# Kernel tuning notes

Hardware: AMD Instinct MI355X
Metric: run time of the kernel (lower is better)

Reference implementation:

```python
import jax, jax.numpy as jnp
import numpy as np

NVFP4_VALUES = jnp.array([0.0, 0.5, 1.0, 1.5, 2.0, 3.0, 4.0, 6.0], dtype=jnp.float32)
NVFP4_MAX = 6.0


def quantize_to_nvfp4(t):
    """Fake-quantize to NVFP4 (e2m1) via nearest codebook magnitude.
    Returns (quantized_tensor, inv_scale) matching the torch reference."""
    amax = jnp.maximum(jnp.max(jnp.abs(t)), 1e-12)
    scale = NVFP4_MAX / amax                      # scalar
    scaled = jnp.clip(t.astype(jnp.float32) * scale, -NVFP4_MAX, NVFP4_MAX)
    signs = jnp.sign(scaled)
    # distance to each of the 8 e2m1 magnitudes -> nearest index
    dist = jnp.abs(jnp.abs(scaled)[..., None] - NVFP4_VALUES)  # (..., 8)
    idx = jnp.argmin(dist, axis=-1)
    quantized = signs * NVFP4_VALUES[idx]
    return quantized, 1.0 / scale


def setup_inputs() -> dict:
    key = jax.random.key(0)
    kx, kw = jax.random.split(key)
    x = jax.random.normal(kx, (512, 4096), dtype=jnp.float32)          # batch=512 (in SUPPORTED_BATCH_SIZES -> no padding)
    # kaiming-uniform-ish init for weight [out_features, in_features]
    bound = float(np.sqrt(6.0 / 4096.0))
    weight = jax.random.uniform(kw, (4096, 4096), dtype=jnp.float32,
                                minval=-bound, maxval=bound)
    return {"x": x, "weight": weight}


def reference(x, weight):
    # batch==512 is an exact supported size, so pad/unpad is identity.
    x_q, x_inv_scale = quantize_to_nvfp4(x)
    w_q, w_inv_scale = quantize_to_nvfp4(weight)
    # out[b,o] = sum_i (x_q*x_s)[b,i] * (w_q*w_s)[o,i]
    out = jnp.einsum('bi,oi->bo', x_q * x_inv_scale, w_q * w_inv_scale)
    return out.astype(x.dtype)
```

## Files before the change

### kernel.cpp

```cpp
#include <hip/hip_runtime.h>

#define M_DIM 512
#define N_DIM 4096
#define K_DIM 4096

typedef __attribute__((ext_vector_type(4))) float f32x4;
typedef __attribute__((ext_vector_type(8))) int i32x8;
typedef __attribute__((ext_vector_type(4))) int i32x4;

#define PART_X_OFF 0
#define PART_X_N   256
#define PART_W_OFF 256
#define PART_W_N   1024
#define AMAX_OFF   1280
#define XQ_BYTE_OFF 8192
#define WQ_BYTE_OFF (XQ_BYTE_OFF + M_DIM * K_DIM)

__global__ __launch_bounds__(256) void amax_kernel(
    const float4* __restrict__ x4, const float4* __restrict__ w4,
    float* __restrict__ ws_f) {
    const int b = blockIdx.x;
    float m = 0.0f;
    if (b < PART_X_N) {
        const int n4 = M_DIM * K_DIM / 4, stride = PART_X_N * 256;
        for (int i = b * 256 + threadIdx.x; i < n4; i += stride) {
            float4 a = x4[i];
            m = fmaxf(m, fmaxf(fmaxf(fabsf(a.x), fabsf(a.y)),
                               fmaxf(fabsf(a.z), fabsf(a.w))));
        }
    } else {
        const int n4 = N_DIM * K_DIM / 4, stride = PART_W_N * 256;
        for (int i = (b - PART_X_N) * 256 + threadIdx.x; i < n4; i += stride) {
            float4 a = w4[i];
            m = fmaxf(m, fmaxf(fmaxf(fabsf(a.x), fabsf(a.y)),
                               fmaxf(fabsf(a.z), fabsf(a.w))));
        }
    }
    for (int off = 32; off > 0; off >>= 1)
        m = fmaxf(m, __shfl_down(m, off, 64));
    __shared__ float sm[4];
    if ((threadIdx.x & 63) == 0) sm[threadIdx.x >> 6] = m;
    __syncthreads();
    if (threadIdx.x == 0) {
        m = fmaxf(fmaxf(sm[0], sm[1]), fmaxf(sm[2], sm[3]));
        ws_f[(b < PART_X_N) ? (PART_X_OFF + b) : (PART_W_OFF + b - PART_X_N)] = m;
    }
}

__device__ __forceinline__ unsigned int q1(float x, float s) {
    float a = fabsf(x) * s;
    unsigned int b;
    if      (a <= 0.25f) b = 0x00u;
    else if (a <= 0.75f) b = 0x30u;
    else if (a <= 1.25f) b = 0x38u;
    else if (a <= 1.75f) b = 0x3Cu;
    else if (a <= 2.5f)  b = 0x40u;
    else if (a <= 3.5f)  b = 0x44u;
    else if (a <= 5.0f)  b = 0x48u;
    else                 b = 0x4Cu;
    return b | ((__float_as_uint(x) >> 24) & 0x80u);
}
__device__ __forceinline__ unsigned int qpack4(float4 v, float s) {
    return q1(v.x, s) | (q1(v.y, s) << 8) | (q1(v.z, s) << 16) | (q1(v.w, s) << 24);
}

__global__ __launch_bounds__(256) void quant_kernel(
    const float4* __restrict__ x4, const float4* __restrict__ w4,
    float* __restrict__ ws_f, unsigned char* __restrict__ ws_b) {
    const int b = blockIdx.x, t = threadIdx.x;
    const bool is_x = b < 512;
    float m = 0.0f;
    if (is_x) {
        m = ws_f[PART_X_OFF + t];
    } else {
        for (int i = t; i < PART_W_N; i += 256)
            m = fmaxf(m, ws_f[PART_W_OFF + i]);
    }
    for (int off = 32; off > 0; off >>= 1)
        m = fmaxf(m, __shfl_down(m, off, 64));
    __shared__ float sm[4];
    if ((t & 63) == 0) sm[t >> 6] = m;
    __syncthreads();
    m = fmaxf(fmaxf(sm[0], sm[1]), fmaxf(sm[2], sm[3]));
    float amax = fmaxf(m, 1e-12f);
    float s = 6.0f / amax;
    if (t == 0 && b == 0)   ws_f[AMAX_OFF + 0] = amax;
    if (t == 0 && b == 512) ws_f[AMAX_OFF + 1] = amax;

    const float4* src = is_x ? x4 : w4;
    unsigned char* dstb = ws_b + (is_x ? XQ_BYTE_OFF : WQ_BYTE_OFF);
    const int idx16 = (is_x ? b : b - 512) * 256 + t;
    const float4* p = src + (size_t)idx16 * 4;
    uint4 o;
    o.x = qpack4(p[0], s);
    o.y = qpack4(p[1], s);
    o.z = qpack4(p[2], s);
    o.w = qpack4(p[3], s);
    ((uint4*)dstb)[idx16] = o;
}

__device__ __forceinline__ void async_copy16(const void* g, void* l) {
    __builtin_amdgcn_global_load_lds(
        (const __attribute__((address_space(1))) unsigned int*)g,
        (__attribute__((address_space(3))) unsigned int*)l, 16, 0, 0);
}

__device__ __forceinline__ i32x8 frag_load(const unsigned char* rowbase,
                                           int mask, int g0) {
    const i32x4 lo = *(const i32x4*)(rowbase + ((g0 ^ mask) * 16));
    const i32x4 hi = *(const i32x4*)(rowbase + (((g0 + 1) ^ mask) * 16));
    return __builtin_shufflevector(lo, hi, 0, 1, 2, 3, 4, 5, 6, 7);
}

__global__ __launch_bounds__(256, 2) void gemm_kernel(
    const unsigned char* __restrict__ A, const unsigned char* __restrict__ B,
    float* __restrict__ C, const float* __restrict__ amax2) {
    __shared__ __align__(16) unsigned char As[64 * 512];
    __shared__ __align__(16) unsigned char Bs[64 * 512];

    const int bid  = blockIdx.x;
    const int bm   = (bid >> 6) * 64;
    const int bn   = ((bid & 7) * 8 + ((bid >> 3) & 7)) * 64;
    const int tid  = threadIdx.x;
    const int lane = tid & 63;
    const int wave = tid >> 6;
    const int wm   = (wave >> 1) * 32;
    const int wn   = (wave & 1) * 32;
    const int t15  = lane & 15;
    const int quad = lane >> 4;

    const float cs = (1.0f / (6.0f / fmaxf(amax2[0], 1e-12f))) *
                     (1.0f / (6.0f / fmaxf(amax2[1], 1e-12f)));

    const unsigned char* agp[8];
    const unsigned char* bgp[8];
#pragma unroll
    for (int j = 0; j < 8; j++) {
        const int c = j * 256 + tid;
        const int row = c >> 5, pcol = c & 31;
        const int gk = pcol ^ (row & 31);
        agp[j] = A + (size_t)(bm + row) * K_DIM + gk * 16;
        bgp[j] = B + (size_t)(bn + row) * K_DIM + gk * 16;
    }

    f32x4 acc[2][2] = {};
    const unsigned char* A0 = As + (size_t)(wm + t15) * 512;
    const unsigned char* A1 = A0 + 16 * 512;
    const unsigned char* B0 = Bs + (size_t)(wn + t15) * 512;
    const unsigned char* B1 = B0 + 16 * 512;
    const int mk0 = t15, mk1 = t15 + 16;

    for (int ko = 0; ko < K_DIM; ko += 512) {
#pragma unroll
        for (int j = 0; j < 8; j++) {
            async_copy16(agp[j] + ko, As + (j * 256 + tid) * 16);
            async_copy16(bgp[j] + ko, Bs + (j * 256 + tid) * 16);
        }
        __syncthreads();

#pragma unroll
        for (int s = 0; s < 4; s++) {
            const int g0 = s * 8 + (quad << 1);
            const i32x8 af0 = frag_load(A0, mk0, g0);
            const i32x8 af1 = frag_load(A1, mk1, g0);
            const i32x8 bf0 = frag_load(B0, mk0, g0);
            const i32x8 bf1 = frag_load(B1, mk1, g0);
            acc[0][0] = __builtin_amdgcn_mfma_scale_f32_16x16x128_f8f6f4(
                af0, bf0, acc[0][0], 0, 0, 0, 0x7F7F7F7F, 0, 0x7F7F7F7F);
            acc[0][1] = __builtin_amdgcn_mfma_scale_f32_16x16x128_f8f6f4(
                af0, bf1, acc[0][1], 0, 0, 0, 0x7F7F7F7F, 0, 0x7F7F7F7F);
            acc[1][0] = __builtin_amdgcn_mfma_scale_f32_16x16x128_f8f6f4(
                af1, bf0, acc[1][0], 0, 0, 0, 0x7F7F7F7F, 0, 0x7F7F7F7F);
            acc[1][1] = __builtin_amdgcn_mfma_scale_f32_16x16x128_f8f6f4(
                af1, bf1, acc[1][1], 0, 0, 0, 0x7F7F7F7F, 0, 0x7F7F7F7F);
        }
        __syncthreads();
    }

#pragma unroll
    for (int i = 0; i < 2; i++)
#pragma unroll
        for (int j = 0; j < 2; j++) {
            const int m0 = bm + wm + i * 16 + quad * 4;
            const int n0 = bn + wn + j * 16 + t15;
#pragma unroll
            for (int r = 0; r < 4; r++)
                C[(size_t)(m0 + r) * N_DIM + n0] = acc[i][j][r] * cs;
        }
}

extern "C" void kernel_launch(void* const* d_in, const int* in_sizes, int n_in,
                              void* d_out, int out_size, void* d_ws, size_t ws_size,
                              hipStream_t stream) {
    const float* x = (const float*)d_in[0];
    const float* w = (const float*)d_in[1];
    float* out = (float*)d_out;

    float* ws_f = (float*)d_ws;
    unsigned char* ws_b = (unsigned char*)d_ws;
    const unsigned char* xq = ws_b + XQ_BYTE_OFF;
    const unsigned char* wq = ws_b + WQ_BYTE_OFF;

    amax_kernel<<<PART_X_N + PART_W_N, 256, 0, stream>>>(
        (const float4*)x, (const float4*)w, ws_f);
    quant_kernel<<<512 + 4096, 256, 0, stream>>>(
        (const float4*)x, (const float4*)w, ws_f, ws_b);
    gemm_kernel<<<(M_DIM / 64) * (N_DIM / 64), 256, 0, stream>>>(
        xq, wq, out, ws_f + AMAX_OFF);
}
```

Before: 133.8 us.

## Pack operands as FP4 nibbles and double-buffer GEMM LDS stages

Quantized operands are now stored as 4-bit e2m1 nibbles instead of 8-bit fp8 encodings, which halves the workspace bytes written by the quant kernel and read by the GEMM. The MFMA scale instruction is switched to FP4 format codes. The GEMM loop moves from a single 512-byte K-stage to 256-byte stages held in two LDS buffers, with the next stage's async copies issued before computing the current one, so loads overlap with MFMA work. This adds manual vmcnt waits and raw barriers, and the correctness of the nibble order and fragment layout depends on the FP4 operand conventions.

```diff
diff --git a/kernel.cpp b/kernel.cpp
--- a/kernel.cpp
+++ b/kernel.cpp
@@ -3,6 +3,7 @@
 #define M_DIM 512
 #define N_DIM 4096
 #define K_DIM 4096
+#define KB    (K_DIM / 2)
 
 typedef __attribute__((ext_vector_type(4))) float f32x4;
 typedef __attribute__((ext_vector_type(8))) int i32x8;
@@ -14,7 +15,7 @@
 #define PART_W_N   1024
 #define AMAX_OFF   1280
 #define XQ_BYTE_OFF 8192
-#define WQ_BYTE_OFF (XQ_BYTE_OFF + M_DIM * K_DIM)
+#define WQ_BYTE_OFF (XQ_BYTE_OFF + M_DIM * KB)
 
 __global__ __launch_bounds__(256) void amax_kernel(
     const float4* __restrict__ x4, const float4* __restrict__ w4,
@@ -47,21 +48,24 @@
     }
 }
 
-__device__ __forceinline__ unsigned int q1(float x, float s) {
+__device__ __forceinline__ unsigned int q1n(float x, float s) {
     float a = fabsf(x) * s;
-    unsigned int b;
-    if      (a <= 0.25f) b = 0x00u;
-    else if (a <= 0.75f) b = 0x30u;
-    else if (a <= 1.25f) b = 0x38u;
-    else if (a <= 1.75f) b = 0x3Cu;
-    else if (a <= 2.5f)  b = 0x40u;
-    else if (a <= 3.5f)  b = 0x44u;
-    else if (a <= 5.0f)  b = 0x48u;
-    else                 b = 0x4Cu;
-    return b | ((__float_as_uint(x) >> 24) & 0x80u);
-}
-__device__ __forceinline__ unsigned int qpack4(float4 v, float s) {
-    return q1(v.x, s) | (q1(v.y, s) << 8) | (q1(v.z, s) << 16) | (q1(v.w, s) << 24);
+    unsigned int c;
+    if      (a <= 0.25f) c = 0u;
+    else if (a <= 0.75f) c = 1u;
+    else if (a <= 1.25f) c = 2u;
+    else if (a <= 1.75f) c = 3u;
+    else if (a <= 2.5f)  c = 4u;
+    else if (a <= 3.5f)  c = 5u;
+    else if (a <= 5.0f)  c = 6u;
+    else                 c = 7u;
+    return c | ((__float_as_uint(x) >> 28) & 0x8u);
+}
+__device__ __forceinline__ unsigned int qpack8(float4 v0, float4 v1, float s) {
+    return  q1n(v0.x, s)        | (q1n(v0.y, s) << 4)  |
+           (q1n(v0.z, s) << 8)  | (q1n(v0.w, s) << 12) |
+           (q1n(v1.x, s) << 16) | (q1n(v1.y, s) << 20) |
+           (q1n(v1.z, s) << 24) | (q1n(v1.w, s) << 28);
 }
 
 __global__ __launch_bounds__(256) void quant_kernel(
@@ -89,14 +93,12 @@
 
     const float4* src = is_x ? x4 : w4;
     unsigned char* dstb = ws_b + (is_x ? XQ_BYTE_OFF : WQ_BYTE_OFF);
-    const int idx16 = (is_x ? b : b - 512) * 256 + t;
-    const float4* p = src + (size_t)idx16 * 4;
-    uint4 o;
-    o.x = qpack4(p[0], s);
-    o.y = qpack4(p[1], s);
-    o.z = qpack4(p[2], s);
-    o.w = qpack4(p[3], s);
-    ((uint4*)dstb)[idx16] = o;
+    const int idx = (is_x ? b : b - 512) * 256 + t;
+    const float4* p = src + (size_t)idx * 4;
+    uint2 o;
+    o.x = qpack8(p[0], p[1], s);
+    o.y = qpack8(p[2], p[3], s);
+    ((uint2*)dstb)[idx] = o;
 }
 
 __device__ __forceinline__ void async_copy16(const void* g, void* l) {
@@ -105,18 +107,18 @@
         (__attribute__((address_space(3))) unsigned int*)l, 16, 0, 0);
 }
 
-__device__ __forceinline__ i32x8 frag_load(const unsigned char* rowbase,
-                                           int mask, int g0) {
-    const i32x4 lo = *(const i32x4*)(rowbase + ((g0 ^ mask) * 16));
-    const i32x4 hi = *(const i32x4*)(rowbase + (((g0 + 1) ^ mask) * 16));
-    return __builtin_shufflevector(lo, hi, 0, 1, 2, 3, 4, 5, 6, 7);
+__device__ __forceinline__ i32x8 frag4(const unsigned char* rowbase,
+                                       int mask, int l) {
+    const i32x4 lo = *(const i32x4*)(rowbase + ((l ^ mask) * 16));
+    const i32x4 z  = {0, 0, 0, 0};
+    return __builtin_shufflevector(lo, z, 0, 1, 2, 3, 4, 5, 6, 7);
 }
 
 __global__ __launch_bounds__(256, 2) void gemm_kernel(
     const unsigned char* __restrict__ A, const unsigned char* __restrict__ B,
     float* __restrict__ C, const float* __restrict__ amax2) {
-    __shared__ __align__(16) unsigned char As[64 * 512];
-    __shared__ __align__(16) unsigned char Bs[64 * 512];
+    __shared__ __align__(16) unsigned char As[2][64 * 256];
+    __shared__ __align__(16) unsigned char Bs[2][64 * 256];
 
     const int bid  = blockIdx.x;
     const int bm   = (bid >> 6) * 64;
@@ -132,50 +134,63 @@
     const float cs = (1.0f / (6.0f / fmaxf(amax2[0], 1e-12f))) *
                      (1.0f / (6.0f / fmaxf(amax2[1], 1e-12f)));
 
-    const unsigned char* agp[8];
-    const unsigned char* bgp[8];
-#pragma unroll
-    for (int j = 0; j < 8; j++) {
+    const unsigned char* agp[4];
+    const unsigned char* bgp[4];
+#pragma unroll
+    for (int j = 0; j < 4; j++) {
         const int c = j * 256 + tid;
-        const int row = c >> 5, pcol = c & 31;
-        const int gk = pcol ^ (row & 31);
-        agp[j] = A + (size_t)(bm + row) * K_DIM + gk * 16;
-        bgp[j] = B + (size_t)(bn + row) * K_DIM + gk * 16;
-    }
+        const int row = c >> 4, pcol = c & 15;
+        const int gk = pcol ^ (row & 15);
+        agp[j] = A + (size_t)(bm + row) * KB + gk * 16;
+        bgp[j] = B + (size_t)(bn + row) * KB + gk * 16;
+    }
+
+#define STAGE(buf, kb)                                                  \
+    do {                                                                \
+        _Pragma("unroll")                                               \
+        for (int j = 0; j < 4; j++) {                                   \
+            async_copy16(agp[j] + (kb), &As[buf][(j * 256 + tid) * 16]);\
+            async_copy16(bgp[j] + (kb), &Bs[buf][(j * 256 + tid) * 16]);\
+        }                                                               \
+    } while (0)
 
     f32x4 acc[2][2] = {};
-    const unsigned char* A0 = As + (size_t)(wm + t15) * 512;
-    const unsigned char* A1 = A0 + 16 * 512;
-    const unsigned char* B0 = Bs + (size_t)(wn + t15) * 512;
-    const unsigned char* B1 = B0 + 16 * 512;
-    const int mk0 = t15, mk1 = t15 + 16;
-
-    for (int ko = 0; ko < K_DIM; ko += 512) {
-#pragma unroll
-        for (int j = 0; j < 8; j++) {
-            async_copy16(agp[j] + ko, As + (j * 256 + tid) * 16);
-            async_copy16(bgp[j] + ko, Bs + (j * 256 + tid) * 16);
-        }
-        __syncthreads();
-
-#pragma unroll
-        for (int s = 0; s < 4; s++) {
-            const int g0 = s * 8 + (quad << 1);
-            const i32x8 af0 = frag_load(A0, mk0, g0);
-            const i32x8 af1 = frag_load(A1, mk1, g0);
-            const i32x8 bf0 = frag_load(B0, mk0, g0);
-            const i32x8 bf1 = frag_load(B1, mk1, g0);
+
+    STAGE(0, 0);
+#pragma unroll 2
+    for (int t = 0; t < 8; ++t) {
+        const int cur = t & 1;
+        if (t < 7) {
+            STAGE(cur ^ 1, (t + 1) * 256);
+            asm volatile("s_waitcnt vmcnt(8)" ::: "memory");
+        } else {
+            asm volatile("s_waitcnt vmcnt(0)" ::: "memory");
+        }
+        __builtin_amdgcn_s_barrier();
+
+        const unsigned char* A0 = As[cur] + (wm + t15) * 256;
+        const unsigned char* A1 = A0 + 16 * 256;
+        const unsigned char* B0 = Bs[cur] + (wn + t15) * 256;
+        const unsigned char* B1 = B0 + 16 * 256;
+#pragma unroll
+        for (int s = 0; s < 4; ++s) {
+            const int l0 = s * 4 + quad;
+            const i32x8 af0 = frag4(A0, t15, l0);
+            const i32x8 af1 = frag4(A1, t15, l0);
+            const i32x8 bf0 = frag4(B0, t15, l0);
+            const i32x8 bf1 = frag4(B1, t15, l0);
             acc[0][0] = __builtin_amdgcn_mfma_scale_f32_16x16x128_f8f6f4(
-                af0, bf0, acc[0][0], 0, 0, 0, 0x7F7F7F7F, 0, 0x7F7F7F7F);
+                af0, bf0, acc[0][0], 4, 4, 0, 0x7F7F7F7F, 0, 0x7F7F7F7F);
             acc[0][1] = __builtin_amdgcn_mfma_scale_f32_16x16x128_f8f6f4(
-                af0, bf1, acc[0][1], 0, 0, 0, 0x7F7F7F7F, 0, 0x7F7F7F7F);
+                af0, bf1, acc[0][1], 4, 4, 0, 0x7F7F7F7F, 0, 0x7F7F7F7F);
             acc[1][0] = __builtin_amdgcn_mfma_scale_f32_16x16x128_f8f6f4(
-                af1, bf0, acc[1][0], 0, 0, 0, 0x7F7F7F7F, 0, 0x7F7F7F7F);
+                af1, bf0, acc[1][0], 4, 4, 0, 0x7F7F7F7F, 0, 0x7F7F7F7F);
             acc[1][1] = __builtin_amdgcn_mfma_scale_f32_16x16x128_f8f6f4(
-                af1, bf1, acc[1][1], 0, 0, 0, 0x7F7F7F7F, 0, 0x7F7F7F7F);
-        }
-        __syncthreads();
-    }
+                af1, bf1, acc[1][1], 4, 4, 0, 0x7F7F7F7F, 0, 0x7F7F7F7F);
+        }
+        __builtin_amdgcn_s_barrier();
+    }
+#undef STAGE
 
 #pragma unroll
     for (int i = 0; i < 2; i++)
```

New measurement: 125.5 us, median of 2. -6.2%, faster.
